# Performance work log

Hardware: AMD Instinct MI355X
Metric: run time of the kernel (lower is better)

The kernel has to match this reference:

```python
import jax, jax.numpy as jnp
import numpy as np

EMBED_DIM = 1024
NUM_HEADS = 16
HEAD_DIM = EMBED_DIM // NUM_HEADS


def setup_inputs() -> dict:
    key = jax.random.key(0)
    ks = jax.random.split(key, 7)
    N, L = 2, 2048
    sv = 1.0 / np.sqrt(HEAD_DIM)
    so = 1.0 / np.sqrt(EMBED_DIM)
    return {
        "values": jax.random.normal(ks[0], (N, L, EMBED_DIM), jnp.float32),
        "keys": jax.random.normal(ks[1], (N, L, EMBED_DIM), jnp.float32),
        "query": jax.random.normal(ks[2], (N, L, EMBED_DIM), jnp.float32),
        # NOTE: original torch code applies self.values to v, k AND q; keys/queries
        # Linears are dead parameters, so only Wv/bv and fc_out are materialized.
        "Wv": jax.random.uniform(ks[3], (HEAD_DIM, HEAD_DIM), jnp.float32, -sv, sv),
        "bv": jax.random.uniform(ks[4], (HEAD_DIM,), jnp.float32, -sv, sv),
        "Wo": jax.random.uniform(ks[5], (EMBED_DIM, EMBED_DIM), jnp.float32, -so, so),
        "bo": jax.random.uniform(ks[6], (EMBED_DIM,), jnp.float32, -so, so),
    }


def reference(values, keys, query, Wv, bv, Wo, bo):
    N, Lq, _ = query.shape
    Lk = keys.shape[1]
    Lv = values.shape[1]
    # split heads: (N, L, H, D)
    v = values.reshape(N, Lv, NUM_HEADS, HEAD_DIM)
    k = keys.reshape(N, Lk, NUM_HEADS, HEAD_DIM)
    q = query.reshape(N, Lq, NUM_HEADS, HEAD_DIM)
    # faithful to source: the SAME value projection is applied to v, k, q
    proj = lambda x: jnp.einsum('nlhd,ed->nlhe', x, Wv) + bv
    v = proj(v)
    k = proj(k)
    q = proj(q)
    # energy: (N, H, Q, K); note scaling by sqrt(embed_dim), as in source
    energy = jnp.einsum('nqhd,nkhd->nhqk', q, k)
    attention = jax.nn.softmax(energy / jnp.sqrt(jnp.float32(EMBED_DIM)), axis=3)
    out = jnp.einsum('nhql,nlhd->nqhd', attention, v).reshape(N, Lq, EMBED_DIM)
    return out @ Wo.T + bo
```

## Files before the change

kernel.cpp:

```cpp
#include <hip/hip_runtime.h>

typedef unsigned short u16;
typedef __bf16 bf16x4 __attribute__((ext_vector_type(4)));
typedef __bf16 bf16x8 __attribute__((ext_vector_type(8)));
typedef float  f32x4  __attribute__((ext_vector_type(4)));
typedef float  f32x16 __attribute__((ext_vector_type(16)));

#define MFMA16(a, b, c) __builtin_amdgcn_mfma_f32_16x16x32_bf16((a), (b), (c), 0, 0, 0)
#define MFMA32(a, b, c) __builtin_amdgcn_mfma_f32_32x32x16_bf16((a), (b), (c), 0, 0, 0)


__global__ __launch_bounds__(256) void conv_wo_kernel(const float* __restrict__ Wo,
                                                      u16* __restrict__ Wob) {
    const int i = (blockIdx.x * 256 + threadIdx.x) * 4;
    float4 v = *(const float4*)&Wo[i];
    bf16x4 o = { (__bf16)v.x, (__bf16)v.y, (__bf16)v.z, (__bf16)v.w };
    *(bf16x4*)&Wob[i] = o;
}

__global__ __launch_bounds__(256) void proj_kernel(
    const float* __restrict__ values, const float* __restrict__ keys,
    const float* __restrict__ query,  const float* __restrict__ Wv,
    const float* __restrict__ bv,
    u16* __restrict__ Qb, u16* __restrict__ Kb, u16* __restrict__ VTb) {
    __shared__ __align__(16) u16 Wvs[64 * 72];
    __shared__ __align__(16) u16 Xs[64 * 72];
    const int b = blockIdx.x;
    const int lt = b & 31, h = (b >> 5) & 15, n = (b >> 9) & 1, t = b >> 10;
    const int nh = n * 16 + h, l0 = lt * 64;
    const int tid = threadIdx.x, wave = tid >> 6, lane = tid & 63;
    const int quad = lane >> 4, l16 = lane & 15;
    const float* xin = (t == 0) ? values : (t == 1 ? keys : query);

#pragma unroll
    for (int j = 0; j < 4; ++j) {
        const int chunk = tid + 256 * j, r = chunk >> 4, c = (chunk & 15) * 4;
        float4 w = *(const float4*)&Wv[r * 64 + c];
        bf16x4 wb = { (__bf16)w.x, (__bf16)w.y, (__bf16)w.z, (__bf16)w.w };
        *(bf16x4*)&Wvs[r * 72 + c] = wb;
        float4 x = *(const float4*)&xin[(size_t)(n * 2048 + l0 + r) * 1024 + h * 64 + c];
        bf16x4 xb = { (__bf16)x.x, (__bf16)x.y, (__bf16)x.z, (__bf16)x.w };
        *(bf16x4*)&Xs[r * 72 + c] = xb;
    }
    __syncthreads();

    bf16x8 wf[4][2], xf[2];
#pragma unroll
    for (int f = 0; f < 4; ++f)
#pragma unroll
        for (int ks = 0; ks < 2; ++ks)
            wf[f][ks] = *(const bf16x8*)&Wvs[(f * 16 + l16) * 72 + ks * 32 + quad * 8];
#pragma unroll
    for (int ks = 0; ks < 2; ++ks)
        xf[ks] = *(const bf16x8*)&Xs[(wave * 16 + l16) * 72 + ks * 32 + quad * 8];

    f32x4 acc[4];
#pragma unroll
    for (int i = 0; i < 4; ++i) acc[i] = (f32x4){0.f, 0.f, 0.f, 0.f};

    if (t == 0) {
#pragma unroll
        for (int nf = 0; nf < 4; ++nf) {
            acc[nf] = MFMA16(xf[0], wf[nf][0], acc[nf]);
            acc[nf] = MFMA16(xf[1], wf[nf][1], acc[nf]);
        }
    } else {
#pragma unroll
        for (int mf = 0; mf < 4; ++mf) {
            acc[mf] = MFMA16(wf[mf][0], xf[0], acc[mf]);
            acc[mf] = MFMA16(wf[mf][1], xf[1], acc[mf]);
        }
    }
    __syncthreads();

    const float scale = (t == 2) ? 0.04508422f : 1.0f;
    if (t == 0) {
#pragma unroll
        for (int nf = 0; nf < 4; ++nf) {
            const float bias = bv[nf * 16 + l16];
            bf16x4 o = { (__bf16)(acc[nf][0] + bias), (__bf16)(acc[nf][1] + bias),
                         (__bf16)(acc[nf][2] + bias), (__bf16)(acc[nf][3] + bias) };
            *(bf16x4*)&Xs[(nf * 16 + l16) * 72 + wave * 16 + quad * 4] = o;
        }
    } else {
#pragma unroll
        for (int mf = 0; mf < 4; ++mf) {
            bf16x4 o = { (__bf16)((acc[mf][0] + bv[mf * 16 + quad * 4 + 0]) * scale),
                         (__bf16)((acc[mf][1] + bv[mf * 16 + quad * 4 + 1]) * scale),
                         (__bf16)((acc[mf][2] + bv[mf * 16 + quad * 4 + 2]) * scale),
                         (__bf16)((acc[mf][3] + bv[mf * 16 + quad * 4 + 3]) * scale) };
            *(bf16x4*)&Xs[(wave * 16 + l16) * 72 + mf * 16 + quad * 4] = o;
        }
    }
    __syncthreads();

    u16* dst = (t == 0) ? VTb : (t == 1 ? Kb : Qb);
#pragma unroll
    for (int j = 0; j < 2; ++j) {
        const int chunk = tid + 256 * j, r = chunk >> 3, c = (chunk & 7) * 8;
        const size_t off = (t == 0) ? (size_t)(nh * 64 + r) * 2048 + l0 + c
                                    : (size_t)(nh * 2048 + l0 + r) * 64 + c;
        *(int4*)&dst[off] = *(const int4*)&Xs[r * 72 + c];
    }
}

__global__ __launch_bounds__(256, 4) void flash_kernel(
    const u16* __restrict__ Qb, const u16* __restrict__ Kb,
    const u16* __restrict__ VTb, float* __restrict__ Opart,
    float* __restrict__ Lp) {
    __shared__ __align__(16) u16 Ks[64 * 72];
    __shared__ __align__(16) u16 Vs[64 * 72];
    __shared__ __align__(16) u16 Ps[4][32 * 72];
    const int b = blockIdx.x;
    const int nh = b >> 5, qsl = (b >> 1) & 15, ks = b & 1;
    const int tid = threadIdx.x, wave = tid >> 6, lane = tid & 63;
    const int l32 = lane & 31, half = lane >> 5;
    const int q0 = qsl * 128 + wave * 32;
    const int s4 = (b >> 1) * 4 + wave;
    u16* Pw = &Ps[wave][0];

    const u16* Qg = Qb + ((size_t)nh * 2048 + q0) * 64;
    bf16x8 qf[4];
#pragma unroll
    for (int kg = 0; kg < 4; ++kg)
        qf[kg] = *(const bf16x8*)&Qg[l32 * 64 + kg * 16 + half * 8];

    f32x16 Oacc[2];
#pragma unroll
    for (int dt = 0; dt < 2; ++dt)
#pragma unroll
        for (int r = 0; r < 16; ++r) Oacc[dt][r] = 0.f;
    float lsum = 0.f;

    const u16* Kg = Kb + (size_t)nh * 2048 * 64;
    const u16* Vg = VTb + (size_t)nh * 64 * 2048;

    for (int kt = 0; kt < 16; ++kt) {
        __syncthreads();
        const int k0 = ks * 1024 + kt * 64;
#pragma unroll
        for (int j = 0; j < 2; ++j) {
            const int chunk = tid + 256 * j, r = chunk >> 3, c = (chunk & 7) * 8;
            *(int4*)&Ks[r * 72 + c] = *(const int4*)&Kg[(size_t)(k0 + r) * 64 + c];
            *(int4*)&Vs[r * 72 + c] = *(const int4*)&Vg[(size_t)r * 2048 + k0 + c];
        }
        __syncthreads();

#pragma unroll
        for (int t2 = 0; t2 < 2; ++t2) {
            f32x16 s;
#pragma unroll
            for (int r = 0; r < 16; ++r) s[r] = 0.f;
#pragma unroll
            for (int kg = 0; kg < 4; ++kg) {
                bf16x8 ak = *(const bf16x8*)&Ks[(t2 * 32 + l32) * 72 + kg * 16 + half * 8];
                s = MFMA32(ak, qf[kg], s);
            }
#pragma unroll
            for (int a = 0; a < 4; ++a) {
                const float p0 = __builtin_amdgcn_exp2f(s[4 * a + 0]);
                const float p1 = __builtin_amdgcn_exp2f(s[4 * a + 1]);
                const float p2 = __builtin_amdgcn_exp2f(s[4 * a + 2]);
                const float p3 = __builtin_amdgcn_exp2f(s[4 * a + 3]);
                lsum += (p0 + p1) + (p2 + p3);
                bf16x4 pk = { (__bf16)p0, (__bf16)p1, (__bf16)p2, (__bf16)p3 };
                *(bf16x4*)&Pw[l32 * 72 + t2 * 32 + a * 8 + half * 4] = pk;
            }
        }

#pragma unroll
        for (int kk = 0; kk < 4; ++kk) {
            bf16x8 bp = *(const bf16x8*)&Pw[l32 * 72 + kk * 16 + half * 8];
#pragma unroll
            for (int dt = 0; dt < 2; ++dt) {
                bf16x8 av = *(const bf16x8*)&Vs[(dt * 32 + l32) * 72 + kk * 16 + half * 8];
                Oacc[dt] = MFMA32(av, bp, Oacc[dt]);
            }
        }
    }

    float* Ob = Opart + ((size_t)s4 * 2 + ks) * 2048;
#pragma unroll
    for (int dt = 0; dt < 2; ++dt)
#pragma unroll
        for (int r = 0; r < 16; ++r)
            Ob[(dt * 16 + r) * 64 + lane] = Oacc[dt][r];
    Lp[((size_t)s4 * 2 + ks) * 64 + lane] = lsum;
}

__global__ __launch_bounds__(256) void combine_kernel(
    const float* __restrict__ Opart, const float* __restrict__ Lp,
    u16* __restrict__ AOb) {
    const int s4 = blockIdx.x;
    const int nh = s4 >> 6, qsl = (s4 >> 2) & 15, w = s4 & 3;
    const int t = threadIdx.x, q = t >> 3, dg = t & 7;
    const int dt = dg >> 2, a = dg & 3;

    const size_t b0 = (size_t)s4 * 2 * 2048;
    const float ls = Lp[(size_t)s4 * 2 * 64 + q] + Lp[(size_t)s4 * 2 * 64 + 32 + q]
                   + Lp[((size_t)s4 * 2 + 1) * 64 + q] + Lp[((size_t)s4 * 2 + 1) * 64 + 32 + q];
    const float inv = 1.0f / ls;

    bf16x8 o;
#pragma unroll
    for (int i = 0; i < 8; ++i) {
        const int r = 4 * a + (i & 3), hf = i >> 2;
        const size_t off = (size_t)(dt * 16 + r) * 64 + hf * 32 + q;
        o[i] = (__bf16)((Opart[b0 + off] + Opart[b0 + 2048 + off]) * inv);
    }
    const int row = (nh >> 4) * 2048 + qsl * 128 + w * 32 + q;
    const int col = (nh & 15) * 64 + dg * 8;
    *(bf16x8*)&AOb[(size_t)row * 1024 + col] = o;
}

__global__ __launch_bounds__(256) void out_gemm_kernel(
    const u16* __restrict__ A, const u16* __restrict__ Bw,
    const float* __restrict__ bo, float* __restrict__ out) {
    __shared__ __align__(16) u16 As[64 * 72];
    __shared__ __align__(16) u16 Bs[64 * 72];
    const int b = blockIdx.x, rt = b >> 4, ct = b & 15;
    const int row0 = rt * 64, col0 = ct * 64;
    const int tid = threadIdx.x, wave = tid >> 6, lane = tid & 63;
    const int quad = lane >> 4, l16 = lane & 15;

    f32x4 acc[4];
#pragma unroll
    for (int i = 0; i < 4; ++i) acc[i] = (f32x4){0.f, 0.f, 0.f, 0.f};

    for (int kt = 0; kt < 16; ++kt) {
        __syncthreads();
        const int k0 = kt * 64;
#pragma unroll
        for (int j = 0; j < 2; ++j) {
            const int chunk = tid + 256 * j, r = chunk >> 3, c = (chunk & 7) * 8;
            *(int4*)&As[r * 72 + c] = *(const int4*)&A[(size_t)(row0 + r) * 1024 + k0 + c];
            *(int4*)&Bs[r * 72 + c] = *(const int4*)&Bw[(size_t)(col0 + r) * 1024 + k0 + c];
        }
        __syncthreads();
#pragma unroll
        for (int ks = 0; ks < 2; ++ks) {
            bf16x8 af = *(const bf16x8*)&As[(wave * 16 + l16) * 72 + ks * 32 + quad * 8];
#pragma unroll
            for (int fc = 0; fc < 4; ++fc) {
                bf16x8 bfr = *(const bf16x8*)&Bs[(fc * 16 + l16) * 72 + ks * 32 + quad * 8];
                acc[fc] = MFMA16(af, bfr, acc[fc]);
            }
        }
    }

#pragma unroll
    for (int fc = 0; fc < 4; ++fc) {
        const float bias = bo[col0 + fc * 16 + l16];
        const int row = row0 + wave * 16 + quad * 4;
        const int col = col0 + fc * 16 + l16;
#pragma unroll
        for (int r = 0; r < 4; ++r)
            out[(size_t)(row + r) * 1024 + col] = acc[fc][r] + bias;
    }
}

extern "C" void kernel_launch(void* const* d_in, const int* in_sizes, int n_in,
                              void* d_out, int out_size, void* d_ws, size_t ws_size,
                              hipStream_t stream) {
    (void)in_sizes; (void)n_in; (void)out_size; (void)ws_size;
    const float* values = (const float*)d_in[0];
    const float* keys   = (const float*)d_in[1];
    const float* query  = (const float*)d_in[2];
    const float* Wv     = (const float*)d_in[3];
    const float* bv     = (const float*)d_in[4];
    const float* Wo     = (const float*)d_in[5];
    const float* bo     = (const float*)d_in[6];

    char* ws = (char*)d_ws;
    u16*   Qb    = (u16*)(ws);
    u16*   Kb    = (u16*)(ws + (8ull  << 20));
    u16*   VTb   = (u16*)(ws + (16ull << 20));
    u16*   AOb   = (u16*)(ws + (24ull << 20));
    u16*   Wob   = (u16*)(ws + (32ull << 20));
    float* Opart = (float*)(ws + (34ull << 20));
    float* Lp    = (float*)(ws + (66ull << 20));

    conv_wo_kernel<<<1024, 256, 0, stream>>>(Wo, Wob);
    proj_kernel<<<3072, 256, 0, stream>>>(values, keys, query, Wv, bv, Qb, Kb, VTb);
    flash_kernel<<<1024, 256, 0, stream>>>(Qb, Kb, VTb, Opart, Lp);
    combine_kernel<<<2048, 256, 0, stream>>>(Opart, Lp, AOb);
    out_gemm_kernel<<<1024, 256, 0, stream>>>(AOb, Wob, bo, (float*)d_out);
}
```

Measured before the change: 191.7 us.

## Read K/V directly from global in flash kernel; stage combine through LDS

The flash kernel drops its shared-memory K and V tiles and the two block barriers per iteration, so each wave loads its MFMA operands straight from global memory and relies on the cache for reuse across waves. This removes the LDS staging and the barriers, but the V^T reads are strided by 2048 elements per row and every wave now issues its own global loads. Separately, the combine kernel reads both partial outputs with coalesced float4 loads, sums them, scatters the result into a padded LDS tile, and then reads it back in the transposed order. This replaces the earlier scattered scalar global reads.

```diff
diff --git a/kernel.cpp b/kernel.cpp
--- a/kernel.cpp
+++ b/kernel.cpp
@@ -108,14 +108,12 @@
     const u16* __restrict__ Qb, const u16* __restrict__ Kb,
     const u16* __restrict__ VTb, float* __restrict__ Opart,
     float* __restrict__ Lp) {
-    __shared__ __align__(16) u16 Ks[64 * 72];
-    __shared__ __align__(16) u16 Vs[64 * 72];
     __shared__ __align__(16) u16 Ps[4][32 * 72];
     const int b = blockIdx.x;
-    const int nh = b >> 5, qsl = (b >> 1) & 15, ks = b & 1;
+    const int nh = b >> 5, ks = b & 1;
     const int tid = threadIdx.x, wave = tid >> 6, lane = tid & 63;
     const int l32 = lane & 31, half = lane >> 5;
-    const int q0 = qsl * 128 + wave * 32;
+    const int q0 = ((b >> 1) & 15) * 128 + wave * 32;
     const int s4 = (b >> 1) * 4 + wave;
     u16* Pw = &Ps[wave][0];
 
@@ -136,15 +134,7 @@
     const u16* Vg = VTb + (size_t)nh * 64 * 2048;
 
     for (int kt = 0; kt < 16; ++kt) {
-        __syncthreads();
         const int k0 = ks * 1024 + kt * 64;
-#pragma unroll
-        for (int j = 0; j < 2; ++j) {
-            const int chunk = tid + 256 * j, r = chunk >> 3, c = (chunk & 7) * 8;
-            *(int4*)&Ks[r * 72 + c] = *(const int4*)&Kg[(size_t)(k0 + r) * 64 + c];
-            *(int4*)&Vs[r * 72 + c] = *(const int4*)&Vg[(size_t)r * 2048 + k0 + c];
-        }
-        __syncthreads();
 
 #pragma unroll
         for (int t2 = 0; t2 < 2; ++t2) {
@@ -153,7 +143,7 @@
             for (int r = 0; r < 16; ++r) s[r] = 0.f;
 #pragma unroll
             for (int kg = 0; kg < 4; ++kg) {
-                bf16x8 ak = *(const bf16x8*)&Ks[(t2 * 32 + l32) * 72 + kg * 16 + half * 8];
+                bf16x8 ak = *(const bf16x8*)&Kg[(size_t)(k0 + t2 * 32 + l32) * 64 + kg * 16 + half * 8];
                 s = MFMA32(ak, qf[kg], s);
             }
 #pragma unroll
@@ -173,7 +163,7 @@
             bf16x8 bp = *(const bf16x8*)&Pw[l32 * 72 + kk * 16 + half * 8];
 #pragma unroll
             for (int dt = 0; dt < 2; ++dt) {
-                bf16x8 av = *(const bf16x8*)&Vs[(dt * 32 + l32) * 72 + kk * 16 + half * 8];
+                bf16x8 av = *(const bf16x8*)&Vg[(size_t)(dt * 32 + l32) * 2048 + k0 + kk * 16 + half * 8];
                 Oacc[dt] = MFMA32(av, bp, Oacc[dt]);
             }
         }
@@ -191,23 +181,34 @@
 __global__ __launch_bounds__(256) void combine_kernel(
     const float* __restrict__ Opart, const float* __restrict__ Lp,
     u16* __restrict__ AOb) {
+    __shared__ __align__(16) float Ls[64 * 36];
     const int s4 = blockIdx.x;
     const int nh = s4 >> 6, qsl = (s4 >> 2) & 15, w = s4 & 3;
-    const int t = threadIdx.x, q = t >> 3, dg = t & 7;
-    const int dt = dg >> 2, a = dg & 3;
-
+    const int t = threadIdx.x;
     const size_t b0 = (size_t)s4 * 2 * 2048;
+
+#pragma unroll
+    for (int jj = 0; jj < 2; ++jj) {
+        const int fi = t + jj * 256;
+        float4 a = *(const float4*)&Opart[b0 + (size_t)fi * 4];
+        float4 c = *(const float4*)&Opart[b0 + 2048 + (size_t)fi * 4];
+        float4 sum = { a.x + c.x, a.y + c.y, a.z + c.z, a.w + c.w };
+        const int flat = fi * 4, i = flat >> 6, lb = flat & 63;
+        const int q = lb & 31, hf = lb >> 5, dtv = i >> 4, r = i & 15;
+        const int d = (r & 3) + 8 * (r >> 2) + 4 * hf + 32 * dtv;
+        *(float4*)&Ls[d * 36 + q] = sum;
+    }
+    __syncthreads();
+
+    const int q = t >> 3, dg = t & 7;
     const float ls = Lp[(size_t)s4 * 2 * 64 + q] + Lp[(size_t)s4 * 2 * 64 + 32 + q]
                    + Lp[((size_t)s4 * 2 + 1) * 64 + q] + Lp[((size_t)s4 * 2 + 1) * 64 + 32 + q];
     const float inv = 1.0f / ls;
 
     bf16x8 o;
 #pragma unroll
-    for (int i = 0; i < 8; ++i) {
-        const int r = 4 * a + (i & 3), hf = i >> 2;
-        const size_t off = (size_t)(dt * 16 + r) * 64 + hf * 32 + q;
-        o[i] = (__bf16)((Opart[b0 + off] + Opart[b0 + 2048 + off]) * inv);
-    }
+    for (int i = 0; i < 8; ++i)
+        o[i] = (__bf16)(Ls[(dg * 8 + i) * 36 + q] * inv);
     const int row = (nh >> 4) * 2048 + qsl * 128 + w * 32 + q;
     const int col = (nh & 15) * 64 + dg * 8;
     *(bf16x8*)&AOb[(size_t)row * 1024 + col] = o;
```

New measurement: 263.8 us. 1.38x slower.
